# Performance work log

Hardware: AMD Instinct MI355X
Metric: run time of the kernel (lower is better)

## Reference

```python
import jax, jax.numpy as jnp
import numpy as np
import math

B, S, D, H, NL, DFF, C, K = 32, 1024, 512, 8, 6, 2048, 128, 8
HD = D // H  # head_dim = 64
EPS = 1e-5


def setup_inputs() -> dict:
    key = jax.random.key(0)
    ks = jax.random.split(key, 24)
    n = lambda k, shape, s=0.02: jax.random.normal(k, shape, jnp.float32) * s
    return {
        'theta': jax.random.uniform(ks[0], (B, S), jnp.float32, -math.pi, math.pi),
        'cond': jax.random.normal(ks[1], (B, C), jnp.float32),
        'attn_bias': jax.random.normal(ks[2], (H, S, S), jnp.float32) * 0.1,
        'embed_W': n(ks[3], (2, D)), 'embed_b': jnp.zeros((D,), jnp.float32),
        'ln1_g': jnp.ones((NL, D), jnp.float32), 'ln1_b': jnp.zeros((NL, D), jnp.float32),
        'ada1_W': n(ks[4], (NL, C, 2 * D)), 'ada1_b': jnp.zeros((NL, 2 * D), jnp.float32),
        'Wq': n(ks[5], (NL, D, D)), 'bq': jnp.zeros((NL, D), jnp.float32),
        'Wk': n(ks[6], (NL, D, D)), 'bk': jnp.zeros((NL, D), jnp.float32),
        'Wv': n(ks[7], (NL, D, D)), 'bv': jnp.zeros((NL, D), jnp.float32),
        'Wo': n(ks[8], (NL, D, D)), 'bo': jnp.zeros((NL, D), jnp.float32),
        'ln2_g': jnp.ones((NL, D), jnp.float32), 'ln2_b': jnp.zeros((NL, D), jnp.float32),
        'ada2_W': n(ks[9], (NL, C, 2 * D)), 'ada2_b': jnp.zeros((NL, 2 * D), jnp.float32),
        'W1': n(ks[10], (NL, D, DFF)), 'b1': jnp.zeros((NL, DFF), jnp.float32),
        'W2': n(ks[11], (NL, DFF, D)), 'b2': jnp.zeros((NL, D), jnp.float32),
        'fn_g': jnp.ones((D,), jnp.float32), 'fn_b': jnp.zeros((D,), jnp.float32),
        'head_W': n(ks[12], (D, 3 * K)), 'head_b': jnp.zeros((3 * K,), jnp.float32),
    }


def _layer_norm(x, g, b):
    m = jnp.mean(x, axis=-1, keepdims=True)
    v = jnp.mean(jnp.square(x - m), axis=-1, keepdims=True)
    return (x - m) * jax.lax.rsqrt(v + EPS) * g + b


def _adaln(x, cond, g, b, pW, pb):
    # AdaLN(x, c) = (1 + scale(c)) * LN(x) + shift(c)
    ss = cond @ pW + pb                      # [B, 2D]
    scale, shift = jnp.split(ss, 2, axis=-1)  # each [B, D]
    return (1.0 + scale[:, None, :]) * _layer_norm(x, g, b) + shift[:, None, :]


def reference(theta, cond, attn_bias, embed_W, embed_b, ln1_g, ln1_b, ada1_W, ada1_b,
              Wq, bq, Wk, bk, Wv, bv, Wo, bo, ln2_g, ln2_b, ada2_W, ada2_b,
              W1, b1, W2, b2, fn_g, fn_b, head_W, head_b):
    b_sz, s_len = theta.shape
    # circular embedding: (cos, sin) -> d_model
    emb_in = jnp.stack([jnp.cos(theta), jnp.sin(theta)], axis=-1)  # [B, S, 2]
    x = emb_in @ embed_W + embed_b                                 # [B, S, D]
    causal = jnp.triu(jnp.ones((s_len, s_len), bool), k=1)         # True above diag
    neg_inf = jnp.asarray(-jnp.inf, x.dtype)
    inv_sqrt = 1.0 / math.sqrt(HD)
    for i in range(NL):
        h = _adaln(x, cond, ln1_g[i], ln1_b[i], ada1_W[i], ada1_b[i])
        q = (h @ Wq[i] + bq[i]).reshape(b_sz, s_len, H, HD)
        k = (h @ Wk[i] + bk[i]).reshape(b_sz, s_len, H, HD)
        v = (h @ Wv[i] + bv[i]).reshape(b_sz, s_len, H, HD)
        scores = jnp.einsum('bqhd,bkhd->bhqk', q, k) * inv_sqrt  # [B, H, S, S]
        scores = scores + attn_bias[None]
        scores = jnp.where(causal[None, None], neg_inf, scores)
        attn = jax.nn.softmax(scores, axis=-1)
        ao = jnp.einsum('bhqk,bkhd->bqhd', attn, v).reshape(b_sz, s_len, D)
        x = x + (ao @ Wo[i] + bo[i])
        h2 = _adaln(x, cond, ln2_g[i], ln2_b[i], ada2_W[i], ada2_b[i])
        ff = jax.nn.gelu(h2 @ W1[i] + b1[i], approximate=False) @ W2[i] + b2[i]
        x = x + ff
    x = _layer_norm(x, fn_g, fn_b)
    return x @ head_W + head_b  # [B, S, 3K] mixture params (logw, mu, log-kappa)
```

## Files before the change

kernel.cpp:

```cpp
#include <hip/hip_runtime.h>


typedef short s8v __attribute__((ext_vector_type(8)));
typedef float f4v __attribute__((ext_vector_type(4)));
typedef unsigned u2v __attribute__((ext_vector_type(2)));
typedef unsigned u4v __attribute__((ext_vector_type(4)));

static __device__ __forceinline__ short f2bf(float f) {
  union { float f; unsigned u; } v; v.f = f;
  unsigned r = v.u + 0x7fffu + ((v.u >> 16) & 1u);
  return (short)(r >> 16);
}
static __device__ __forceinline__ float bf2f(unsigned short s) {
  union { unsigned u; float f; } v; v.u = ((unsigned)s) << 16;
  return v.f;
}
static __device__ __forceinline__ unsigned cvtpk(float lo, float hi) {
  unsigned r;
  asm("v_cvt_pk_bf16_f32 %0, %1, %2" : "=v"(r) : "v"(lo), "v"(hi));
  return r;
}
static __device__ __forceinline__ void gl_lds16(const short* g, short* l) {
  __builtin_amdgcn_global_load_lds(
      (const __attribute__((address_space(1))) unsigned int*)g,
      (__attribute__((address_space(3))) unsigned int*)l, 16, 0, 0);
}

__global__ void transpose_all_k(const float* __restrict__ Wq, const float* __restrict__ Wk,
                                const float* __restrict__ Wv, const float* __restrict__ Wo,
                                const float* __restrict__ W1, const float* __restrict__ W2,
                                int l, short* __restrict__ wbf) {
  int id = blockIdx.x;
  const float* in; short* out; int K, N, tx, ty;
  if (id < 1024) {
    int m = id >> 8, t = id & 255;
    in = (m == 0 ? Wq : m == 1 ? Wk : m == 2 ? Wv : Wo) + (size_t)l * 262144;
    out = wbf + (size_t)m * 262144;
    K = 512; N = 512; tx = t & 15; ty = t >> 4;
  } else if (id < 2048) {
    int t = id - 1024;
    in = W1 + (size_t)l * 1048576; out = wbf + 1048576;
    K = 512; N = 2048; tx = t & 63; ty = t >> 6;
  } else {
    int t = id - 2048;
    in = W2 + (size_t)l * 1048576; out = wbf + 2097152;
    K = 2048; N = 512; tx = t & 15; ty = t >> 4;
  }
  __shared__ float tb[32][33];
  int n0 = tx * 32, k0 = ty * 32;
  int cx = threadIdx.x & 31, cy = threadIdx.x >> 5;
#pragma unroll
  for (int r = 0; r < 4; r++)
    tb[cy + r * 8][cx] = in[(size_t)(k0 + cy + r * 8) * N + n0 + cx];
  __syncthreads();
#pragma unroll
  for (int r = 0; r < 4; r++)
    out[(size_t)(n0 + cy + r * 8) * K + k0 + cx] = f2bf(tb[cx][cy + r * 8]);
}

__global__ void bias_cvt_k(const float* __restrict__ in, short* __restrict__ out) {
  int i = blockIdx.x * 256 + threadIdx.x;
  float4 v = ((const float4*)in)[i];
  ushort4 o;
  o.x = (unsigned short)f2bf(v.x);
  o.y = (unsigned short)f2bf(v.y);
  o.z = (unsigned short)f2bf(v.z);
  o.w = (unsigned short)f2bf(v.w);
  ((ushort4*)out)[i] = o;
}

__global__ void hwt_k(const float* __restrict__ hW, short* __restrict__ hWT) {
  int i = blockIdx.x * 256 + threadIdx.x;
  int n = i >> 9, k = i & 511;
  hWT[i] = (n < 24) ? f2bf(hW[(size_t)k * 24 + n]) : (short)0;
}

__global__ void concat_qkvb_k(const float* bq, const float* bk, const float* bv, float* out) {
  int l = blockIdx.x;
  for (int i = threadIdx.x; i < 1536; i += 256) {
    float v = (i < 512) ? bq[l * 512 + i] * 0.125f
            : (i < 1024 ? bk[l * 512 + i - 512] : bv[l * 512 + i - 1024]);
    out[l * 1536 + i] = v;
  }
}

__global__ void cond_proj_k(const float* __restrict__ cond,
                            const float* __restrict__ a1W, const float* __restrict__ a1b,
                            const float* __restrict__ a2W, const float* __restrict__ a2b,
                            float* __restrict__ ss) {
  int lw = blockIdx.y, which = lw & 1, l = lw >> 1;
  const float* W = (which ? a2W : a1W) + (size_t)l * 128 * 1024;
  const float* bb = (which ? a2b : a1b) + (size_t)l * 1024;
  __shared__ float cs[32 * 128];
  for (int i = threadIdx.x; i < 32 * 128; i += 256) cs[i] = cond[i];
  __syncthreads();
  int n = blockIdx.x * 256 + threadIdx.x;
  float bias = bb[n];
  for (int g = 0; g < 4; g++) {
    float acc[8];
#pragma unroll
    for (int i = 0; i < 8; i++) acc[i] = 0.f;
    for (int c = 0; c < 128; c++) {
      float w = W[(size_t)c * 1024 + n];
#pragma unroll
      for (int i = 0; i < 8; i++) acc[i] += cs[(g * 8 + i) * 128 + c] * w;
    }
#pragma unroll
    for (int i = 0; i < 8; i++)
      ss[((size_t)lw * 32 + g * 8 + i) * 1024 + n] = acc[i] + bias;
  }
}

__global__ void embed_k(const float* __restrict__ theta, const float* __restrict__ eW,
                        const float* __restrict__ eb, float* __restrict__ x) {
  int row = blockIdx.x * 4 + (threadIdx.x >> 6), lane = threadIdx.x & 63;
  float th = theta[row], sn, cn;
  sincosf(th, &sn, &cn);
  int d = lane * 8;
  float* xo = x + (size_t)row * 512 + d;
#pragma unroll
  for (int i = 0; i < 8; i++) xo[i] = cn * eW[d + i] + sn * eW[512 + d + i] + eb[d + i];
}

template<bool HASDEL>
__global__ void adaln_k(float* __restrict__ x, const short* delta,
                        const float* __restrict__ ss,
                        const float* __restrict__ g, const float* __restrict__ be,
                        short* h) {
  int row = blockIdx.x * 4 + (threadIdx.x >> 6), lane = threadIdx.x & 63;
  int b = row >> 10;
  float* xr = x + (size_t)row * 512 + lane * 8;
  float4 va = ((const float4*)xr)[0], vb = ((const float4*)xr)[1];
  float v[8] = {va.x, va.y, va.z, va.w, vb.x, vb.y, vb.z, vb.w};
  if (HASDEL) {
    s8v dv = *(const s8v*)(delta + (size_t)row * 512 + lane * 8);
#pragma unroll
    for (int i = 0; i < 8; i++) v[i] += bf2f((unsigned short)dv[i]);
    float4 o0 = {v[0], v[1], v[2], v[3]}, o1 = {v[4], v[5], v[6], v[7]};
    ((float4*)xr)[0] = o0; ((float4*)xr)[1] = o1;
  }
  float sm = 0.f;
#pragma unroll
  for (int i = 0; i < 8; i++) sm += v[i];
#pragma unroll
  for (int off = 1; off < 64; off <<= 1) sm += __shfl_xor(sm, off);
  float mean = sm * (1.f / 512.f);
  float sq = 0.f;
#pragma unroll
  for (int i = 0; i < 8; i++) { float d = v[i] - mean; sq += d * d; }
#pragma unroll
  for (int off = 1; off < 64; off <<= 1) sq += __shfl_xor(sq, off);
  float rs = rsqrtf(sq * (1.f / 512.f) + 1e-5f);
  const float* sb = ss + (size_t)b * 1024 + lane * 8;
  const float* gp = g + lane * 8;
  const float* bp = be + lane * 8;
  s8v o;
#pragma unroll
  for (int i = 0; i < 8; i++) {
    float xh = (v[i] - mean) * rs * gp[i] + bp[i];
    o[i] = f2bf((1.f + sb[i]) * xh + sb[i + 512]);
  }
  *(s8v*)(h + (size_t)row * 512 + lane * 8) = o;
}

__global__ void fln_k(const float* __restrict__ x, const short* delta,
                      const float* __restrict__ g, const float* __restrict__ be,
                      short* h) {
  int row = blockIdx.x * 4 + (threadIdx.x >> 6), lane = threadIdx.x & 63;
  const float* xr = x + (size_t)row * 512 + lane * 8;
  float4 va = ((const float4*)xr)[0], vb = ((const float4*)xr)[1];
  float v[8] = {va.x, va.y, va.z, va.w, vb.x, vb.y, vb.z, vb.w};
  s8v dv = *(const s8v*)(delta + (size_t)row * 512 + lane * 8);
#pragma unroll
  for (int i = 0; i < 8; i++) v[i] += bf2f((unsigned short)dv[i]);
  float sm = 0.f;
#pragma unroll
  for (int i = 0; i < 8; i++) sm += v[i];
#pragma unroll
  for (int off = 1; off < 64; off <<= 1) sm += __shfl_xor(sm, off);
  float mean = sm * (1.f / 512.f);
  float sq = 0.f;
#pragma unroll
  for (int i = 0; i < 8; i++) { float d = v[i] - mean; sq += d * d; }
#pragma unroll
  for (int off = 1; off < 64; off <<= 1) sq += __shfl_xor(sq, off);
  float rs = rsqrtf(sq * (1.f / 512.f) + 1e-5f);
  const float* gp = g + lane * 8;
  const float* bp = be + lane * 8;
  s8v o;
#pragma unroll
  for (int i = 0; i < 8; i++) o[i] = f2bf((v[i] - mean) * rs * gp[i] + bp[i]);
  *(s8v*)(h + (size_t)row * 512 + lane * 8) = o;
}

template<int EPI>
__global__ __launch_bounds__(256) void gemm_bt_k(const short* __restrict__ A,
                                                 const short* __restrict__ BT,
                                                 const float* __restrict__ bias,
                                                 short* __restrict__ outb,
                                                 int N, int K) {
  __shared__ __align__(16) short lsA[2][4096];
  __shared__ __align__(16) short lsB[2][4096];
  int tid = threadIdx.x, lane = tid & 63, w = tid >> 6;
  int wm = w >> 1, wn = w & 1;
  int l15 = lane & 15, l4 = lane >> 4;
  int lrow = lane >> 2, lchunk = lane & 3;
  int poff = ((l15 << 2) + (l4 ^ ((l15 >> 1) & 3))) << 3;
  int nb = N >> 7;
  int bid = blockIdx.x;
  int xcd = bid & 7, rr = bid >> 3;
  int mloc = rr / nb, nidx = rr - mloc * nb;
  int m0 = (xcd * 32 + mloc) << 7, n0 = nidx << 7;

  f4v z4 = {0.f, 0.f, 0.f, 0.f};
  f4v acc[4][4];
#pragma unroll
  for (int i = 0; i < 4; i++)
#pragma unroll
    for (int j = 0; j < 4; j++) acc[i][j] = z4;

  int co = (lchunk ^ ((lrow >> 1) & 3)) << 3;

  auto STAGE = [&](int t) {
    int slot = t & 1;
    int ko = t << 5;
#pragma unroll
    for (int tt = 0; tt < 2; tt++) {
      int r0 = w * 32 + tt * 16;
      int row = r0 + lrow;
      gl_lds16(A + (size_t)(m0 + row) * K + ko + co, lsA[slot] + r0 * 32);
      gl_lds16(BT + (size_t)(n0 + row) * K + ko + co, lsB[slot] + r0 * 32);
    }
  };

  int NT = K >> 5;
  STAGE(0);
  for (int t = 0; t < NT; ++t) {
    if (t + 1 < NT) {
      STAGE(t + 1);
      asm volatile("s_waitcnt vmcnt(4)" ::: "memory");
    } else {
      asm volatile("s_waitcnt vmcnt(0)" ::: "memory");
    }
    __builtin_amdgcn_s_barrier();
    int slot = t & 1;
    const short* At = lsA[slot] + (wm * 4) * 512 + poff;
    const short* Bt = lsB[slot] + (wn * 4) * 512 + poff;
    s8v af[4], bfr[4];
#pragma unroll
    for (int i = 0; i < 4; i++) {
      af[i] = *(const s8v*)(At + i * 512);
      bfr[i] = *(const s8v*)(Bt + i * 512);
    }
#pragma unroll
    for (int i = 0; i < 4; i++)
#pragma unroll
      for (int j = 0; j < 4; j++)
        acc[i][j] = __builtin_amdgcn_mfma_f32_16x16x32_bf16(af[i], bfr[j], acc[i][j], 0, 0, 0);
    __builtin_amdgcn_s_barrier();
  }
#pragma unroll
  for (int i = 0; i < 4; i++) {
    int gr0 = m0 + wm * 64 + i * 16 + l4 * 4;
#pragma unroll
    for (int j = 0; j < 4; j++) {
      int gc = n0 + wn * 64 + j * 16 + l15;
      float bv = bias[gc];
#pragma unroll
      for (int r = 0; r < 4; r++) {
        float v = acc[i][j][r] + bv;
        if (EPI == 1) {
          float tg = v * (-1.5957691216f - 0.0713548162726f * v * v);
          v = v / (1.f + __expf(tg));
        }
        outb[(size_t)(gr0 + r) * N + gc] = f2bf(v);
      }
    }
  }
}

__global__ __launch_bounds__(256) void qkvt_k(const short* __restrict__ A,
                                              const short* __restrict__ BT,
                                              const float* __restrict__ bias,
                                              short* __restrict__ qk,
                                              short* __restrict__ vtb) {
  __shared__ __align__(16) short lsA[2][4096];
  __shared__ __align__(16) short lsB[2][4096];
  int tid = threadIdx.x, lane = tid & 63, w = tid >> 6;
  int wm = w >> 1, wn = w & 1;
  int l15 = lane & 15, l4 = lane >> 4;
  int lrow = lane >> 2, lchunk = lane & 3;
  int poff = ((l15 << 2) + (l4 ^ ((l15 >> 1) & 3))) << 3;
  int bid = blockIdx.x;
  int xcd = bid & 7, rr = bid >> 3;
  int mloc = rr / 12, nidx = rr - mloc * 12;
  int m0 = (xcd * 32 + mloc) << 7, n0 = nidx << 7;
  bool isV = (n0 >= 1024);
  bool isQ = (n0 < 512);

  f4v z4 = {0.f, 0.f, 0.f, 0.f};
  f4v acc[4][4];
#pragma unroll
  for (int i = 0; i < 4; i++)
#pragma unroll
    for (int j = 0; j < 4; j++) acc[i][j] = z4;

  int co = (lchunk ^ ((lrow >> 1) & 3)) << 3;

  auto STAGE = [&](int t) {
    int slot = t & 1;
    int ko = t << 5;
#pragma unroll
    for (int tt = 0; tt < 2; tt++) {
      int r0 = w * 32 + tt * 16;
      int row = r0 + lrow;
      gl_lds16(A + (size_t)(m0 + row) * 512 + ko + co, lsA[slot] + r0 * 32);
      gl_lds16(BT + (size_t)(n0 + row) * 512 + ko + co, lsB[slot] + r0 * 32);
    }
  };

  const int NT = 16;
  STAGE(0);
  for (int t = 0; t < NT; ++t) {
    if (t + 1 < NT) {
      STAGE(t + 1);
      asm volatile("s_waitcnt vmcnt(4)" ::: "memory");
    } else {
      asm volatile("s_waitcnt vmcnt(0)" ::: "memory");
    }
    __builtin_amdgcn_s_barrier();
    int slot = t & 1;
    const short* At = lsA[slot] + (wm * 4) * 512 + poff;
    const short* Bt = lsB[slot] + (wn * 4) * 512 + poff;
    s8v af[4], bfr[4];
#pragma unroll
    for (int i = 0; i < 4; i++) {
      af[i] = *(const s8v*)(At + i * 512);
      bfr[i] = *(const s8v*)(Bt + i * 512);
    }
    if (!isV) {
#pragma unroll
      for (int i = 0; i < 4; i++)
#pragma unroll
        for (int j = 0; j < 4; j++)
          acc[i][j] = __builtin_amdgcn_mfma_f32_16x16x32_bf16(af[i], bfr[j], acc[i][j], 0, 0, 0);
    } else {
#pragma unroll
      for (int j = 0; j < 4; j++)
#pragma unroll
        for (int i = 0; i < 4; i++)
          acc[j][i] = __builtin_amdgcn_mfma_f32_16x16x32_bf16(bfr[j], af[i], acc[j][i], 0, 0, 0);
    }
    __builtin_amdgcn_s_barrier();
  }
  if (!isV) {
    float scl = isQ ? 0.125f : 1.f;
#pragma unroll
    for (int i = 0; i < 4; i++) {
      int gr0 = m0 + wm * 64 + i * 16 + l4 * 4;
#pragma unroll
      for (int j = 0; j < 4; j++) {
        int gc = n0 + wn * 64 + j * 16 + l15;
        float bv = bias[gc];
#pragma unroll
        for (int r = 0; r < 4; r++)
          qk[(size_t)(gr0 + r) * 1024 + gc] = f2bf(acc[i][j][r] * scl + bv);
      }
    }
  } else {
    int b = m0 >> 10, s0 = m0 & 1023;
#pragma unroll
    for (int j = 0; j < 4; j++) {
      int col = n0 + wn * 64 + j * 16 + l4 * 4;
#pragma unroll
      for (int i = 0; i < 4; i++) {
        int scol = s0 + wm * 64 + i * 16 + l15;
#pragma unroll
        for (int r = 0; r < 4; r++) {
          float v = acc[j][i][r] + bias[col + r];
          vtb[((size_t)b * 512 + col - 1024 + r) * 1024 + scol] = f2bf(v);
        }
      }
    }
  }
}

__global__ __launch_bounds__(256, 4) void attn_k(const short* __restrict__ qk,
                                                 const short* __restrict__ vt,
                                                 const short* __restrict__ biasNT,
                                                 short* __restrict__ ao) {
  __shared__ __align__(16) short Kl[2][64 * 64];
  __shared__ __align__(16) short Vl[2][64 * 64];
  int tid = threadIdx.x, lane = tid & 63, w = tid >> 6;
  int bid = blockIdx.x;
  int qt = 7 - (bid >> 8), b = (bid >> 3) & 31, h = bid & 7;
  int l15 = lane & 15, l4 = lane >> 4;
  int lrow = lane >> 3, lchunk = lane & 7;

  f4v z4 = {0.f, 0.f, 0.f, 0.f};
  s8v qf[2][2];
#pragma unroll
  for (int g = 0; g < 2; g++) {
    const short* qp = qk + (size_t)(b * 1024 + qt * 128 + g * 64 + w * 16 + l15) * 1024 + h * 64;
    qf[g][0] = *(const s8v*)(qp + l4 * 8);
    qf[g][1] = *(const s8v*)(qp + 32 + l4 * 8);
  }
  f4v o[2][4], lac[2];
#pragma unroll
  for (int g = 0; g < 2; g++) {
    lac[g] = z4;
#pragma unroll
    for (int j = 0; j < 4; j++) o[g][j] = z4;
  }
  s8v ones;
#pragma unroll
  for (int e = 0; e < 8; e++) ones[e] = (short)0x3F80;

  auto STAGE = [&](int buf, int kt) {
#pragma unroll
    for (int t = 0; t < 2; t++) {
      int r0 = (w * 2 + t) * 8;
      int row = r0 + lrow;
      gl_lds16(qk + (size_t)(b * 1024 + kt * 64 + row) * 1024 + 512 + h * 64 +
                   ((lchunk ^ (row & 7)) << 3),
               &Kl[buf][r0 * 64]);
      gl_lds16(vt + (size_t)(b * 512 + h * 64 + row) * 1024 + kt * 64 +
                   ((lchunk ^ (row & 7)) << 3),
               &Vl[buf][r0 * 64]);
    }
  };

  int nkt = 2 * qt + 2;
  STAGE(0, 0);
  for (int kt = 0; kt < nkt; kt++) {
    int cur = kt & 1;
    ushort4 bh[2][4];
#pragma unroll
    for (int g = 0; g < 2; g++) {
      if (kt > 2 * qt + g) continue;
      const short* bp = biasNT + ((size_t)h * 1024 + qt * 128 + g * 64 + w * 16 + l15) * 1024 +
                        kt * 64 + l4 * 4;
#pragma unroll
      for (int j = 0; j < 4; j++) bh[g][j] = *(const ushort4*)(bp + j * 16);
    }
    __builtin_amdgcn_sched_barrier(0);
    if (kt + 1 < nkt) {
      STAGE(cur ^ 1, kt + 1);
      asm volatile("s_waitcnt vmcnt(4)" ::: "memory");
    } else {
      asm volatile("s_waitcnt vmcnt(0)" ::: "memory");
    }
    __builtin_amdgcn_s_barrier();
    const short* Kc = &Kl[cur][0];
    const short* Vc = &Vl[cur][0];
#pragma unroll
    for (int g = 0; g < 2; g++) {
      int diag = 2 * qt + g;
      if (kt > diag) continue;
      f4v s[4];
#pragma unroll
      for (int j = 0; j < 4; j++) {
        f4v bc;
        bc[0] = bf2f(bh[g][j].x); bc[1] = bf2f(bh[g][j].y);
        bc[2] = bf2f(bh[g][j].z); bc[3] = bf2f(bh[g][j].w);
        int kr = j * 16 + l15;
        s8v kf0 = *(const s8v*)(Kc + kr * 64 + ((l4 ^ (kr & 7)) << 3));
        s8v kf1 = *(const s8v*)(Kc + kr * 64 + (((l4 + 4) ^ (kr & 7)) << 3));
        s[j] = __builtin_amdgcn_mfma_f32_16x16x32_bf16(kf0, qf[g][0], bc, 0, 0, 0);
        s[j] = __builtin_amdgcn_mfma_f32_16x16x32_bf16(kf1, qf[g][1], s[j], 0, 0, 0);
      }
      if (kt == diag) {
#pragma unroll
        for (int j = 0; j < 4; j++)
#pragma unroll
          for (int r = 0; r < 4; r++) {
            int kk = j * 16 + l4 * 4 + r, qq = w * 16 + l15;
            s[j][r] = (kk > qq) ? 0.f : __expf(s[j][r]);
          }
      } else {
#pragma unroll
        for (int j = 0; j < 4; j++)
#pragma unroll
          for (int r = 0; r < 4; r++) s[j][r] = __expf(s[j][r]);
      }
      unsigned X0[4], X1[4];
#pragma unroll
      for (int j = 0; j < 4; j++) {
        X0[j] = cvtpk(s[j][0], s[j][1]);
        X1[j] = cvtpk(s[j][2], s[j][3]);
      }
      u2v a0 = __builtin_amdgcn_permlane32_swap(X0[0], X0[1], false, false);
      u2v a1 = __builtin_amdgcn_permlane16_swap(a0[0], a0[1], false, false);
      u2v b0 = __builtin_amdgcn_permlane32_swap(X1[0], X1[1], false, false);
      u2v b1 = __builtin_amdgcn_permlane16_swap(b0[0], b0[1], false, false);
      u2v c0 = __builtin_amdgcn_permlane32_swap(X0[2], X0[3], false, false);
      u2v c1 = __builtin_amdgcn_permlane16_swap(c0[0], c0[1], false, false);
      u2v d0 = __builtin_amdgcn_permlane32_swap(X1[2], X1[3], false, false);
      u2v d1 = __builtin_amdgcn_permlane16_swap(d0[0], d0[1], false, false);
      u4v P0 = {a1[0], b1[0], a1[1], b1[1]};
      u4v P1 = {c1[0], d1[0], c1[1], d1[1]};
      s8v pf0 = __builtin_bit_cast(s8v, P0);
      s8v pf1 = __builtin_bit_cast(s8v, P1);
      lac[g] = __builtin_amdgcn_mfma_f32_16x16x32_bf16(pf0, ones, lac[g], 0, 0, 0);
      lac[g] = __builtin_amdgcn_mfma_f32_16x16x32_bf16(pf1, ones, lac[g], 0, 0, 0);
#pragma unroll
      for (int j = 0; j < 4; j++) {
        int dr = j * 16 + l15;
        s8v vf0 = *(const s8v*)(Vc + dr * 64 + ((l4 ^ (dr & 7)) << 3));
        s8v vf1 = *(const s8v*)(Vc + dr * 64 + (((l4 + 4) ^ (dr & 7)) << 3));
        o[g][j] = __builtin_amdgcn_mfma_f32_16x16x32_bf16(pf0, vf0, o[g][j], 0, 0, 0);
        o[g][j] = __builtin_amdgcn_mfma_f32_16x16x32_bf16(pf1, vf1, o[g][j], 0, 0, 0);
      }
    }
    __builtin_amdgcn_s_barrier();
  }
#pragma unroll
  for (int g = 0; g < 2; g++)
#pragma unroll
    for (int r = 0; r < 4; r++) {
      float rl = 1.f / lac[g][r];
      int qr = qt * 128 + g * 64 + w * 16 + l4 * 4 + r;
#pragma unroll
      for (int j = 0; j < 4; j++) {
        int d = j * 16 + l15;
        ao[(size_t)(b * 1024 + qr) * 512 + h * 64 + d] = f2bf(o[g][j][r] * rl);
      }
    }
}

__global__ __launch_bounds__(256) void head_k(const short* __restrict__ X,
                                              const short* __restrict__ hWT,
                                              const float* __restrict__ hb,
                                              float* __restrict__ out) {
  __shared__ __align__(16) short lA[128 * 64];
  int tid = threadIdx.x, lane = tid & 63, w = tid >> 6;
  int l15 = lane & 15, l4 = lane >> 4;
  int lrow = lane >> 3, lchunk = lane & 7;
  int m0 = blockIdx.x * 128;
  f4v z4 = {0.f, 0.f, 0.f, 0.f};
  f4v acc[2][2];
#pragma unroll
  for (int i = 0; i < 2; i++)
#pragma unroll
    for (int j = 0; j < 2; j++) acc[i][j] = z4;

  for (int k0 = 0; k0 < 512; k0 += 64) {
#pragma unroll
    for (int t = 0; t < 4; t++) {
      int r0 = (w * 4 + t) * 8;
      int row = r0 + lrow;
      gl_lds16(X + (size_t)(m0 + row) * 512 + k0 + ((lchunk ^ (row & 7)) << 3), lA + r0 * 64);
    }
    __syncthreads();
#pragma unroll
    for (int kk = 0; kk < 2; kk++) {
      s8v af[2], bfr[2];
#pragma unroll
      for (int i = 0; i < 2; i++) {
        int ra = w * 32 + i * 16 + l15;
        af[i] = *(const s8v*)(lA + ra * 64 + (((l4 + kk * 4) ^ (ra & 7)) << 3));
      }
#pragma unroll
      for (int j = 0; j < 2; j++)
        bfr[j] = *(const s8v*)(hWT + (size_t)(j * 16 + l15) * 512 + k0 + kk * 32 + l4 * 8);
#pragma unroll
      for (int i = 0; i < 2; i++)
#pragma unroll
        for (int j = 0; j < 2; j++)
          acc[i][j] = __builtin_amdgcn_mfma_f32_16x16x32_bf16(af[i], bfr[j], acc[i][j], 0, 0, 0);
    }
    __syncthreads();
  }
#pragma unroll
  for (int i = 0; i < 2; i++) {
#pragma unroll
    for (int j = 0; j < 2; j++) {
      int col = j * 16 + l15;
      if (col < 24) {
        float bv = hb[col];
#pragma unroll
        for (int r = 0; r < 4; r++) {
          int row = m0 + w * 32 + i * 16 + l4 * 4 + r;
          out[(size_t)row * 24 + col] = acc[i][j][r] + bv;
        }
      }
    }
  }
}

extern "C" void kernel_launch(void* const* d_in, const int* in_sizes, int n_in,
                              void* d_out, int out_size, void* d_ws, size_t ws_size,
                              hipStream_t stream) {
  (void)in_sizes; (void)n_in; (void)out_size;
  const float* theta   = (const float*)d_in[0];
  const float* cond    = (const float*)d_in[1];
  const float* attn_b  = (const float*)d_in[2];
  const float* embed_W = (const float*)d_in[3];
  const float* embed_b = (const float*)d_in[4];
  const float* ln1_g   = (const float*)d_in[5];
  const float* ln1_b   = (const float*)d_in[6];
  const float* ada1_W  = (const float*)d_in[7];
  const float* ada1_b  = (const float*)d_in[8];
  const float* Wq      = (const float*)d_in[9];
  const float* bq      = (const float*)d_in[10];
  const float* Wk      = (const float*)d_in[11];
  const float* bk      = (const float*)d_in[12];
  const float* Wv      = (const float*)d_in[13];
  const float* bv      = (const float*)d_in[14];
  const float* Wo      = (const float*)d_in[15];
  const float* bo      = (const float*)d_in[16];
  const float* ln2_g   = (const float*)d_in[17];
  const float* ln2_b   = (const float*)d_in[18];
  const float* ada2_W  = (const float*)d_in[19];
  const float* ada2_b  = (const float*)d_in[20];
  const float* W1      = (const float*)d_in[21];
  const float* b1      = (const float*)d_in[22];
  const float* W2      = (const float*)d_in[23];
  const float* b2      = (const float*)d_in[24];
  const float* fn_g    = (const float*)d_in[25];
  const float* fn_b    = (const float*)d_in[26];
  const float* head_W  = (const float*)d_in[27];
  const float* head_b  = (const float*)d_in[28];

  const size_t REQ = 242814976ull;
  const size_t REQ2 = 259592192ull;
  if (ws_size < REQ) return;
  bool bias_once = (ws_size >= REQ2);

  char* ws = (char*)d_ws;
  float* xw    = (float*)(ws + 0ull);
  short* qk    = (short*)(ws + 67108864ull);
  short* vtb   = (short*)(ws + 134217728ull);
  short* biasT = (short*)(ws + (bias_once ? 242814976ull : 167772160ull));
  short* qf    = (short*)(ws + 67108864ull);
  short* hbuf  = (short*)(ws + 201326592ull);
  short* wbf   = (short*)(ws + 234881024ull);
  float* ssb   = (float*)(ws + 241172480ull);
  float* bqkv  = (float*)(ws + 242745344ull);
  short* hWT   = (short*)(ws + 242782208ull);

  concat_qkvb_k<<<6, 256, 0, stream>>>(bq, bk, bv, bqkv);
  cond_proj_k<<<dim3(4, 12), 256, 0, stream>>>(cond, ada1_W, ada1_b, ada2_W, ada2_b, ssb);
  hwt_k<<<64, 256, 0, stream>>>(head_W, hWT);
  embed_k<<<8192, 256, 0, stream>>>(theta, embed_W, embed_b, xw);
  if (bias_once) bias_cvt_k<<<8192, 256, 0, stream>>>(attn_b, biasT);

  for (int l = 0; l < 6; l++) {
    transpose_all_k<<<3072, 256, 0, stream>>>(Wq, Wk, Wv, Wo, W1, W2, l, wbf);
    if (!bias_once) bias_cvt_k<<<8192, 256, 0, stream>>>(attn_b, biasT);

    if (l == 0)
      adaln_k<false><<<8192, 256, 0, stream>>>(xw, nullptr, ssb + (size_t)(l * 2) * 32768,
                                               ln1_g + l * 512, ln1_b + l * 512, hbuf);
    else
      adaln_k<true><<<8192, 256, 0, stream>>>(xw, hbuf, ssb + (size_t)(l * 2) * 32768,
                                              ln1_g + l * 512, ln1_b + l * 512, hbuf);
    qkvt_k<<<3072, 256, 0, stream>>>(hbuf, wbf, bqkv + l * 1536, qk, vtb);
    attn_k<<<2048, 256, 0, stream>>>(qk, vtb, biasT, hbuf);
    gemm_bt_k<0><<<1024, 256, 0, stream>>>(hbuf, wbf + 786432, bo + l * 512, vtb, 512, 512);
    adaln_k<true><<<8192, 256, 0, stream>>>(xw, vtb, ssb + (size_t)(l * 2 + 1) * 32768,
                                            ln2_g + l * 512, ln2_b + l * 512, hbuf);
    gemm_bt_k<1><<<4096, 256, 0, stream>>>(hbuf, wbf + 1048576, b1 + l * 2048, qf, 2048, 512);
    gemm_bt_k<0><<<1024, 256, 0, stream>>>(qf, wbf + 2097152, b2 + l * 512, hbuf, 512, 2048);
  }
  fln_k<<<8192, 256, 0, stream>>>(xw, hbuf, fn_g, fn_b, hbuf);
  head_k<<<256, 256, 0, stream>>>(hbuf, hWT, head_b, (float*)d_out);
}
```

Before: 2.827 ms.

## Triple-buffer LDS in GEMM kernels and prefetch fragments across iterations

Both bf16 GEMM kernels (generic and QKV) move from a double-buffered to a triple-buffered LDS pipeline. Global-to-LDS loads are issued two K-steps ahead, and the next step's register fragments are read before the loop continues. This leaves one barrier per iteration instead of two, so global load latency and LDS reads can overlap with MFMA work. LDS use per block rises from 32KB to 48KB and a launch_bounds occupancy hint of 3 is added, which may reduce resident blocks or add register pressure.

```diff
diff --git a/kernel.cpp b/kernel.cpp
--- a/kernel.cpp
+++ b/kernel.cpp
@@ -194,13 +194,13 @@
 }
 
 template<int EPI>
-__global__ __launch_bounds__(256) void gemm_bt_k(const short* __restrict__ A,
-                                                 const short* __restrict__ BT,
-                                                 const float* __restrict__ bias,
-                                                 short* __restrict__ outb,
-                                                 int N, int K) {
-  __shared__ __align__(16) short lsA[2][4096];
-  __shared__ __align__(16) short lsB[2][4096];
+__global__ __launch_bounds__(256, 3) void gemm_bt_k(const short* __restrict__ A,
+                                                    const short* __restrict__ BT,
+                                                    const float* __restrict__ bias,
+                                                    short* __restrict__ outb,
+                                                    int N, int K) {
+  __shared__ __align__(16) short lsA[3][4096];
+  __shared__ __align__(16) short lsB[3][4096];
   int tid = threadIdx.x, lane = tid & 63, w = tid >> 6;
   int wm = w >> 1, wn = w & 1;
   int l15 = lane & 15, l4 = lane >> 4;
@@ -222,7 +222,7 @@
   int co = (lchunk ^ ((lrow >> 1) & 3)) << 3;
 
   auto STAGE = [&](int t) {
-    int slot = t & 1;
+    int slot = t % 3;
     int ko = t << 5;
 #pragma unroll
     for (int tt = 0; tt < 2; tt++) {
@@ -232,32 +232,37 @@
       gl_lds16(BT + (size_t)(n0 + row) * K + ko + co, lsB[slot] + r0 * 32);
     }
   };
-
-  int NT = K >> 5;
-  STAGE(0);
-  for (int t = 0; t < NT; ++t) {
-    if (t + 1 < NT) {
-      STAGE(t + 1);
-      asm volatile("s_waitcnt vmcnt(4)" ::: "memory");
-    } else {
-      asm volatile("s_waitcnt vmcnt(0)" ::: "memory");
-    }
-    __builtin_amdgcn_s_barrier();
-    int slot = t & 1;
+  auto LOADF = [&](int t, s8v* af, s8v* bfr) {
+    int slot = t % 3;
     const short* At = lsA[slot] + (wm * 4) * 512 + poff;
     const short* Bt = lsB[slot] + (wn * 4) * 512 + poff;
-    s8v af[4], bfr[4];
 #pragma unroll
     for (int i = 0; i < 4; i++) {
       af[i] = *(const s8v*)(At + i * 512);
       bfr[i] = *(const s8v*)(Bt + i * 512);
     }
+  };
+
+  int NT = K >> 5;
+  STAGE(0); STAGE(1);
+  asm volatile("s_waitcnt vmcnt(4)" ::: "memory");
+  __builtin_amdgcn_s_barrier();
+  s8v af[4], bfr[4];
+  LOADF(0, af, bfr);
+  for (int t = 0; t < NT; ++t) {
+    if (t + 2 < NT) STAGE(t + 2);
+    __builtin_amdgcn_sched_barrier(0);
 #pragma unroll
     for (int i = 0; i < 4; i++)
 #pragma unroll
       for (int j = 0; j < 4; j++)
         acc[i][j] = __builtin_amdgcn_mfma_f32_16x16x32_bf16(af[i], bfr[j], acc[i][j], 0, 0, 0);
-    __builtin_amdgcn_s_barrier();
+    if (t + 1 < NT) {
+      if (t + 2 < NT) asm volatile("s_waitcnt vmcnt(4)" ::: "memory");
+      else            asm volatile("s_waitcnt vmcnt(0)" ::: "memory");
+      __builtin_amdgcn_s_barrier();
+      LOADF(t + 1, af, bfr);
+    }
   }
 #pragma unroll
   for (int i = 0; i < 4; i++) {
@@ -279,13 +284,13 @@
   }
 }
 
-__global__ __launch_bounds__(256) void qkvt_k(const short* __restrict__ A,
-                                              const short* __restrict__ BT,
-                                              const float* __restrict__ bias,
-                                              short* __restrict__ qk,
-                                              short* __restrict__ vtb) {
-  __shared__ __align__(16) short lsA[2][4096];
-  __shared__ __align__(16) short lsB[2][4096];
+__global__ __launch_bounds__(256, 3) void qkvt_k(const short* __restrict__ A,
+                                                 const short* __restrict__ BT,
+                                                 const float* __restrict__ bias,
+                                                 short* __restrict__ qk,
+                                                 short* __restrict__ vtb) {
+  __shared__ __align__(16) short lsA[3][4096];
+  __shared__ __align__(16) short lsB[3][4096];
   int tid = threadIdx.x, lane = tid & 63, w = tid >> 6;
   int wm = w >> 1, wn = w & 1;
   int l15 = lane & 15, l4 = lane >> 4;
@@ -308,7 +313,7 @@
   int co = (lchunk ^ ((lrow >> 1) & 3)) << 3;
 
   auto STAGE = [&](int t) {
-    int slot = t & 1;
+    int slot = t % 3;
     int ko = t << 5;
 #pragma unroll
     for (int tt = 0; tt < 2; tt++) {
@@ -318,26 +323,26 @@
       gl_lds16(BT + (size_t)(n0 + row) * 512 + ko + co, lsB[slot] + r0 * 32);
     }
   };
-
-  const int NT = 16;
-  STAGE(0);
-  for (int t = 0; t < NT; ++t) {
-    if (t + 1 < NT) {
-      STAGE(t + 1);
-      asm volatile("s_waitcnt vmcnt(4)" ::: "memory");
-    } else {
-      asm volatile("s_waitcnt vmcnt(0)" ::: "memory");
-    }
-    __builtin_amdgcn_s_barrier();
-    int slot = t & 1;
+  auto LOADF = [&](int t, s8v* af, s8v* bfr) {
+    int slot = t % 3;
     const short* At = lsA[slot] + (wm * 4) * 512 + poff;
     const short* Bt = lsB[slot] + (wn * 4) * 512 + poff;
-    s8v af[4], bfr[4];
 #pragma unroll
     for (int i = 0; i < 4; i++) {
       af[i] = *(const s8v*)(At + i * 512);
       bfr[i] = *(const s8v*)(Bt + i * 512);
     }
+  };
+
+  const int NT = 16;
+  STAGE(0); STAGE(1);
+  asm volatile("s_waitcnt vmcnt(4)" ::: "memory");
+  __builtin_amdgcn_s_barrier();
+  s8v af[4], bfr[4];
+  LOADF(0, af, bfr);
+  for (int t = 0; t < NT; ++t) {
+    if (t + 2 < NT) STAGE(t + 2);
+    __builtin_amdgcn_sched_barrier(0);
     if (!isV) {
 #pragma unroll
       for (int i = 0; i < 4; i++)
@@ -351,7 +356,12 @@
         for (int i = 0; i < 4; i++)
           acc[j][i] = __builtin_amdgcn_mfma_f32_16x16x32_bf16(bfr[j], af[i], acc[j][i], 0, 0, 0);
     }
-    __builtin_amdgcn_s_barrier();
+    if (t + 1 < NT) {
+      if (t + 2 < NT) asm volatile("s_waitcnt vmcnt(4)" ::: "memory");
+      else            asm volatile("s_waitcnt vmcnt(0)" ::: "memory");
+      __builtin_amdgcn_s_barrier();
+      LOADF(t + 1, af, bfr);
+    }
   }
   if (!isV) {
     float scl = isQ ? 0.125f : 1.f;
```

Result: slower. 2.926 ms (+3.5%).
